# Kernel tuning notes

Measured on AMD Instinct MI355X. Metric: run time of the kernel, lower is better.

The kernel has to match this reference:

```python
import itertools
import jax, jax.numpy as jnp
import numpy as np

RES = 14
B = 64
DIM = 384
NH = 8
KD = 32
DV = 128  # attn_ratio * key_dim
SCALE = KD ** -0.5


def _bias_idxs(res):
    points = list(itertools.product(range(res), range(res)))
    offs, idxs = {}, []
    for p1 in points:
        for p2 in points:
            o = (abs(p1[0] - p2[0]), abs(p1[1] - p2[1]))
            if o not in offs:
                offs[o] = len(offs)
            idxs.append(offs[o])
    n = res * res
    return np.asarray(idxs, dtype=np.int32).reshape(n, n), len(offs)


def setup_inputs() -> dict:
    key = jax.random.key(0)
    ks = jax.random.split(key, 16)
    idxs, n_off = _bias_idxs(RES)  # n_off == 196 for res=14
    f = lambda k, shape, s=0.05: jax.random.normal(k, shape, dtype=jnp.float32) * s
    return {
        "x": jax.random.normal(ks[0], (B, DIM, RES, RES), dtype=jnp.float32),
        "qw": f(ks[1], (NH * KD, DIM)), "qb": f(ks[2], (NH * KD,)),
        "kw": f(ks[3], (NH * KD, DIM)), "kb": f(ks[4], (NH * KD,)),
        "vw": f(ks[5], (NH * DV, DIM)), "vb": f(ks[6], (NH * DV,)),
        "vlw": f(ks[7], (NH * DV, 1, 3, 3)), "vlb": f(ks[8], (NH * DV,)),
        "th1_w": f(ks[9], (NH, NH), 0.3), "th1_b": f(ks[10], (NH,)),
        "th2_w": f(ks[11], (NH, NH), 0.3), "th2_b": f(ks[12], (NH,)),
        "projw": f(ks[13], (DIM, NH * DV)), "projb": f(ks[14], (DIM,)),
        "bias_seg": f(ks[15], (NH, n_off), 0.5),
        "bias_idxs": jnp.asarray(idxs),
    }


def reference(x, qw, qb, kw, kb, vw, vb, vlw, vlb,
              th1_w, th1_b, th2_w, th2_b, projw, projb,
              bias_seg, bias_idxs):
    Bb, C, H, W = x.shape
    N = H * W
    xf = x.reshape(Bb, C, N)
    # 1x1 conv (+ folded BN) projections
    q = (jnp.einsum('oc,bcn->bon', qw, xf) + qb[:, None]).reshape(Bb, NH, KD, N).transpose(0, 1, 3, 2)  # [B,h,N,kd]
    k = (jnp.einsum('oc,bcn->bon', kw, xf) + kb[:, None]).reshape(Bb, NH, KD, N)                        # [B,h,kd,N]
    v4 = (jnp.einsum('oc,bcn->bon', vw, xf) + vb[:, None]).reshape(Bb, NH * DV, H, W)
    # depthwise 3x3 local branch (+ folded BN)
    v_local = jax.lax.conv_general_dilated(
        v4, vlw, window_strides=(1, 1), padding=[(1, 1), (1, 1)],
        dimension_numbers=('NCHW', 'OIHW', 'NCHW'), feature_group_count=NH * DV,
    ) + vlb[None, :, None, None]
    v = v4.reshape(Bb, NH, DV, N).transpose(0, 1, 3, 2)  # [B,h,N,dv]
    # attention scores + relative bias (bicubic interp 196->196 is identity)
    attn = jnp.einsum('bhnk,bhkm->bhnm', q, k) * SCALE
    bias = bias_seg[:, bias_idxs]  # [h,N,N]
    attn = attn + bias[None]
    # talking heads (1x1 conv over head dim) -> softmax -> talking heads
    attn = jnp.einsum('hg,bgnm->bhnm', th1_w, attn) + th1_b[None, :, None, None]
    attn = jax.nn.softmax(attn, axis=-1)
    attn = jnp.einsum('hg,bgnm->bhnm', th2_w, attn) + th2_b[None, :, None, None]
    o = jnp.einsum('bhnm,bhmd->bhnd', attn, v)           # [B,h,N,dv]
    o = o.transpose(0, 1, 3, 2).reshape(Bb, NH * DV, H, W) + v_local
    # proj: ReLU -> 1x1 conv (+ folded BN)
    o = jax.nn.relu(o)
    out = jnp.einsum('oc,bchw->bohw', projw, o) + projb[None, :, None, None]
    return out
```

## Files before the change

kernel.cpp:

```cpp
#include <hip/hip_runtime.h>
#include <hip/hip_bf16.h>


#define RES   14
#define NSP   196
#define NHD   8
#define KDIM  32
#define DVV   128
#define DIM   384
#define NQK   256
#define SCALE 0.17677669529663687f
#define SROW  224
#define NSTRIP 13

typedef __attribute__((ext_vector_type(8))) short bf16x8;
typedef __attribute__((ext_vector_type(4))) float f32x4;
typedef __attribute__((ext_vector_type(4))) unsigned short u16x4;
typedef unsigned short u16;
typedef unsigned int u32;

__device__ __forceinline__ u16 f2b(float f) {
    union { __hip_bfloat16 b; u16 u; } c; c.b = __float2bfloat16(f); return c.u;
}
__device__ __forceinline__ float b2f(u16 u) {
    union { __hip_bfloat16 b; u16 u; } c; c.u = u; return __bfloat162float(c.b);
}

__device__ __forceinline__ void gld16(const void* g, void* l) {
    __builtin_amdgcn_global_load_lds(
        (__attribute__((address_space(1))) void*)(unsigned long long)(const char*)g,
        (__attribute__((address_space(3))) void*)l, 16, 0, 0);
}

__device__ __forceinline__ void gemm128_bk64(const char* Aseg, long rbA,
                                             const char* Bseg, long rbB, int kIters,
                                             u16* A_lds, u16* B_lds, f32x4 acc[4][4])
{
    const int tid  = threadIdx.x;
    const int wid  = tid >> 6;
    const int lane = tid & 63;
    const int lrow = lane >> 2;
    const int lcb  = (lane & 3) << 4;
    const int r0   = wid * 32;
    const int wm   = (wid & 1) * 64, wn = (wid >> 1) * 64;
    const int l15  = lane & 15, lq8 = (lane >> 4) * 8;

    #pragma unroll
    for (int i = 0; i < 4; ++i)
        #pragma unroll
        for (int j = 0; j < 4; ++j) acc[i][j] = (f32x4){0.f, 0.f, 0.f, 0.f};

    const char* ap0 = Aseg + (long)(r0 + lrow) * rbA + lcb;
    const char* ap1 = ap0 + 16 * rbA;
    const char* bp0 = Bseg + (long)(r0 + lrow) * rbB + lcb;
    const char* bp1 = bp0 + 16 * rbB;
    u16* la0 = A_lds + r0 * 32;
    u16* la1 = la0 + 512;
    u16* lb0 = B_lds + r0 * 32;
    u16* lb1 = lb0 + 512;

    for (int kk = 0; kk < kIters; ++kk) {
        gld16(ap0, la0);        gld16(ap1, la1);
        gld16(bp0, lb0);        gld16(bp1, lb1);
        gld16(ap0 + 64, la0 + 4096); gld16(ap1 + 64, la1 + 4096);
        gld16(bp0 + 64, lb0 + 4096); gld16(bp1 + 64, lb1 + 4096);
        ap0 += 128; ap1 += 128; bp0 += 128; bp1 += 128;
        __syncthreads();
        #pragma unroll
        for (int s = 0; s < 2; ++s) {
            bf16x8 af[4], bfr[4];
            #pragma unroll
            for (int i = 0; i < 4; ++i)
                af[i] = *(const bf16x8*)&A_lds[s * 4096 + (wm + i * 16 + l15) * 32 + lq8];
            #pragma unroll
            for (int j = 0; j < 4; ++j)
                bfr[j] = *(const bf16x8*)&B_lds[s * 4096 + (wn + j * 16 + l15) * 32 + lq8];
            #pragma unroll
            for (int i = 0; i < 4; ++i)
                #pragma unroll
                for (int j = 0; j < 4; ++j)
                    acc[i][j] = __builtin_amdgcn_mfma_f32_16x16x32_bf16(
                        af[i], bfr[j], acc[i][j], 0, 0, 0);
        }
        __syncthreads();
    }
}

__global__ __launch_bounds__(256) void k_prep(
    const float* __restrict__ qw, const float* __restrict__ kw,
    const float* __restrict__ vw, const float* __restrict__ pw,
    const float* __restrict__ th1w, const float* __restrict__ th1b,
    const float* __restrict__ bias_seg, const float* __restrict__ vlw,
    const float* __restrict__ x,
    u16* __restrict__ wqkv, u16* __restrict__ pwb, float* __restrict__ biasmix,
    u16* __restrict__ wpack, u16* __restrict__ xb)
{
    __shared__ float t[32][33];
    const int bid = blockIdx.x;
    if (bid < 960) {
        const int i = (bid * 256 + threadIdx.x) * 4;
        const float* src; u16* dst;
        if (i < 98304)       { src = qw + i;            dst = wqkv + i; }
        else if (i < 196608) { src = kw + (i - 98304);  dst = wqkv + i; }
        else if (i < 589824) { src = vw + (i - 196608); dst = wqkv + i; }
        else                 { src = pw + (i - 589824); dst = pwb + (i - 589824); }
        float4 v = *(const float4*)src;
        u16x4 o;
        o[0] = f2b(v.x); o[1] = f2b(v.y); o[2] = f2b(v.z); o[3] = f2b(v.w);
        *(u16x4*)dst = o;
    } else if (bid == 960) {
        for (int i2 = threadIdx.x; i2 < 8 * NSP; i2 += 256) {
            int hh = i2 / NSP, off = i2 - hh * NSP;
            float a = th1b[hh];
            #pragma unroll
            for (int g = 0; g < 8; ++g) a += th1w[hh * 8 + g] * bias_seg[g * NSP + off];
            biasmix[i2] = a;
        }
    } else if (bid < 997) {
        int i2 = (bid - 961) * 256 + threadIdx.x;
        if (i2 < 9216) {
            int g = i2 / 72, r = i2 - g * 72;
            int tap = r >> 3, tt = r & 7;
            wpack[i2] = f2b(vlw[(g * 8 + tt) * 9 + tap]);
        }
    } else {
        const int L = bid - 997;
        const int b = L / 84, r = L - b * 84;
        const int c0 = (r / 7) * 32, n0 = (r % 7) * 32;
        const int tx = threadIdx.x & 31, ty = threadIdx.x >> 5;
        #pragma unroll
        for (int l = 0; l < 4; ++l) {
            int c = c0 + ty + 8 * l, n = n0 + tx;
            t[ty + 8 * l][tx] = (n < NSP) ? x[((long)b * DIM + c) * NSP + n] : 0.f;
        }
        __syncthreads();
        #pragma unroll
        for (int l = 0; l < 4; ++l) {
            int n = n0 + ty + 8 * l, c = c0 + tx;
            if (n < NSP) xb[((long)b * NSP + n) * DIM + c] = f2b(t[tx][ty + 8 * l]);
        }
    }
}

__global__ __launch_bounds__(256) void k_qkv(
    const u16* __restrict__ xb, const u16* __restrict__ wqkv,
    const float* __restrict__ qb, const float* __restrict__ kb,
    const float* __restrict__ vb,
    u16* __restrict__ qt, u16* __restrict__ kb16, u16* __restrict__ vt)
{
    __shared__ u16 A_lds[8192], B_lds[8192];
    const int m0 = blockIdx.x * 128, oc0 = blockIdx.y * 128;
    f32x4 acc[4][4];
    gemm128_bk64((const char*)xb + (long)m0 * 768, 768,
                 (const char*)wqkv + (long)oc0 * 768, 768, 6, A_lds, B_lds, acc);

    const int tid = threadIdx.x, wid = tid >> 6, lane = tid & 63;
    const int wm = (wid & 1) * 64, wn = (wid >> 1) * 64;
    const int col = lane & 15, quad = lane >> 4;
    #pragma unroll
    for (int i = 0; i < 4; ++i) {
        #pragma unroll
        for (int j = 0; j < 4; ++j) {
            #pragma unroll
            for (int r = 0; r < 4; ++r) {
                int m  = m0 + wm + i * 16 + quad * 4 + r;
                int oc = oc0 + wn + j * 16 + col;
                int b = m / NSP, n = m - b * NSP;
                float v = acc[i][j][r];
                if (oc < 256) {
                    qt[(long)m * NQK + oc] = f2b(v + qb[oc]);
                } else if (oc < 512) {
                    int o = oc - 256;
                    kb16[(long)m * NQK + o] = f2b(v + kb[o]);
                } else {
                    int o = oc - 512, h = o >> 7, d = o & 127;
                    vt[(((long)b * NHD + h) * NSP + n) * DVV + d] = f2b(v + vb[o]);
                }
            }
        }
    }
}

__global__ __launch_bounds__(256) void k_vtdw(
    const u16* __restrict__ vt, const u16* __restrict__ wpack,
    const float* __restrict__ vlb,
    u16* __restrict__ vtT, u16* __restrict__ vlt)
{
    __shared__ u16 t[32][33];
    const int bid = blockIdx.x;
    if (bid < 14336) {
        const int n_i = bid % 7;
        const int d_i = (bid / 7) & 3;
        const int bh  = bid / 28;
        const int d0 = d_i * 32, n0 = n_i * 32;
        const int tx = threadIdx.x & 31, ty = threadIdx.x >> 5;
        #pragma unroll
        for (int l = 0; l < 4; ++l) {
            int n = n0 + ty + 8 * l, d = d0 + tx;
            t[ty + 8 * l][tx] = (n < NSP) ? vt[((long)bh * NSP + n) * DVV + d] : (u16)0;
        }
        __syncthreads();
        #pragma unroll
        for (int l = 0; l < 4; ++l) {
            int d = d0 + ty + 8 * l, m = n0 + tx;
            vtT[((long)bh * DVV + d) * 224 + m] = t[tx][ty + 8 * l];
        }
    } else {
        const int b2 = bid - 14336;
        const int nx = b2 % 13;
        const int bh = b2 / 13;
        const int tid = threadIdx.x;
        const int dg = tid & 15;
        const int nl = tid >> 4;
        const int n  = nx * 16 + nl;
        if (n >= NSP) return;
        const int d0 = dg * 8;
        const int h  = bh & 7;
        const int y = n / RES, xx = n - y * RES;
        const long plane = (long)bh * NSP * DVV;
        float acc[8];
        #pragma unroll
        for (int k = 0; k < 8; ++k) acc[k] = vlb[h * DVV + d0 + k];
        const u16* wb = wpack + (h * 16 + dg) * 72;
        #pragma unroll
        for (int dy = -1; dy <= 1; ++dy) {
            int yy = y + dy;
            if (yy < 0 || yy >= RES) continue;
            #pragma unroll
            for (int dx = -1; dx <= 1; ++dx) {
                int xn = xx + dx;
                if (xn < 0 || xn >= RES) continue;
                int tap = (dy + 1) * 3 + dx + 1;
                bf16x8 v  = *(const bf16x8*)&vt[plane + (yy * RES + xn) * DVV + d0];
                bf16x8 wv = *(const bf16x8*)&wb[tap * 8];
                #pragma unroll
                for (int k = 0; k < 8; ++k)
                    acc[k] += b2f((u16)wv[k]) * b2f((u16)v[k]);
            }
        }
        bf16x8 r;
        #pragma unroll
        for (int k = 0; k < 8; ++k) r[k] = (short)f2b(acc[k]);
        *(bf16x8*)&vlt[plane + (long)n * DVV + d0] = r;
    }
}

__global__ __launch_bounds__(512, 2) void k_attn2(
    const u16* __restrict__ qt, const u16* __restrict__ kb16,
    const u16* __restrict__ vtT, const u16* __restrict__ vlt,
    const float* __restrict__ th1w, const float* __restrict__ th2w,
    const float* __restrict__ th2b, const float* __restrict__ biasmix,
    u16* __restrict__ ot)
{
    __shared__ u16 S[128 * SROW];
    __shared__ u16 bmS[8 * NSP];
    const int tid = threadIdx.x;
    const int L  = blockIdx.x;
    const int wq = L >> 3;
    const int b  = (L & 7) + ((wq / NSTRIP) << 3);
    const int n0 = (wq % NSTRIP) * 16;
    const int wid = tid >> 6, lane = tid & 63;
    const int l15 = lane & 15, lq8 = (lane >> 4) * 8;
    const int quad = lane >> 4, col = lane & 15;

    for (int i = tid; i < 8 * NSP; i += 512) bmS[i] = f2b(biasmix[i]);
    __syncthreads();

    {
        const long qrow = ((long)(b * NSP) + n0 + l15) * NQK;
        bf16x8 af[8];
        #pragma unroll
        for (int g = 0; g < 8; ++g)
            af[g] = *(const bf16x8*)&qt[qrow + g * 32 + lq8];
        #pragma unroll
        for (int jj = 0; jj < 2; ++jj) {
            const int j = wid + jj * 8;
            if (j >= 13) break;
            const long krow = ((long)(b * NSP) + j * 16 + l15) * NQK;
            f32x4 t[8];
            #pragma unroll
            for (int g = 0; g < 8; ++g) {
                bf16x8 bv = *(const bf16x8*)&kb16[krow + g * 32 + lq8];
                t[g] = __builtin_amdgcn_mfma_f32_16x16x32_bf16(
                    af[g], bv, (f32x4){0.f, 0.f, 0.f, 0.f}, 0, 0, 0);
            }
            const int m = j * 16 + col;
            const int ym = m / RES, xm = m - ym * RES;
            int offr[4];
            #pragma unroll
            for (int r = 0; r < 4; ++r) {
                int gn = n0 + quad * 4 + r;
                int yn = gn / RES, xn = gn - yn * RES;
                int off = abs(yn - ym) * RES + abs(xn - xm);
                offr[r] = (off > 195) ? 195 : off;
            }
            #pragma unroll
            for (int h = 0; h < 8; ++h) {
                float o[4];
                #pragma unroll
                for (int r = 0; r < 4; ++r) o[r] = b2f(bmS[h * NSP + offr[r]]);
                #pragma unroll
                for (int g = 0; g < 8; ++g) {
                    const float w = th1w[h * 8 + g] * SCALE;
                    #pragma unroll
                    for (int r = 0; r < 4; ++r) o[r] += w * t[g][r];
                }
                #pragma unroll
                for (int r = 0; r < 4; ++r)
                    S[(h * 16 + quad * 4 + r) * SROW + m] = f2b(o[r]);
            }
        }
    }
    __syncthreads();

    {
        const int c = lane & 15, rg = lane >> 4;
        #pragma unroll
        for (int it = 0; it < 4; ++it) {
            u16* row = &S[(wid * 16 + it * 4 + rg) * SROW];
            float v[13];
            #pragma unroll
            for (int k = 0; k < 12; ++k) v[k] = b2f(row[c + 16 * k]);
            v[12] = (c < 4) ? b2f(row[192 + c]) : -1e30f;
            float mx = v[0];
            #pragma unroll
            for (int k = 1; k < 13; ++k) mx = fmaxf(mx, v[k]);
            #pragma unroll
            for (int o = 1; o < 16; o <<= 1) mx = fmaxf(mx, __shfl_xor(mx, o));
            float sum = 0.f;
            #pragma unroll
            for (int k = 0; k < 13; ++k) { v[k] = __expf(v[k] - mx); sum += v[k]; }
            if (c >= 4) sum -= v[12];
            #pragma unroll
            for (int o = 1; o < 16; o <<= 1) sum += __shfl_xor(sum, o);
            float inv = 1.0f / sum;
            #pragma unroll
            for (int k = 0; k < 12; ++k) row[c + 16 * k] = f2b(v[k] * inv);
            if (c < 4) row[192 + c] = f2b(v[12] * inv);
        }
    }
    __syncthreads();

    {
        for (int p = tid; p < 16 * 112; p += 512) {
            const int nl = p / 112, kp = p - nl * 112;
            const int m0 = kp * 2;
            if (m0 >= NSP) {
                #pragma unroll
                for (int h = 0; h < 8; ++h)
                    *(u32*)&S[(h * 16 + nl) * SROW + m0] = 0u;
                continue;
            }
            float s0[8], s1[8];
            #pragma unroll
            for (int g = 0; g < 8; ++g) {
                u32 v = *(const u32*)&S[(g * 16 + nl) * SROW + m0];
                s0[g] = b2f((u16)(v & 0xffff));
                s1[g] = b2f((u16)(v >> 16));
            }
            #pragma unroll
            for (int h = 0; h < 8; ++h) {
                float o0 = th2b[h], o1 = th2b[h];
                #pragma unroll
                for (int g = 0; g < 8; ++g) {
                    const float w = th2w[h * 8 + g];
                    o0 += w * s0[g];
                    o1 += w * s1[g];
                }
                *(u32*)&S[(h * 16 + nl) * SROW + m0] =
                    (u32)f2b(o0) | ((u32)f2b(o1) << 16);
            }
        }
    }
    __syncthreads();

    {
        const int h = wid;
        const long vrow = (long)(b * NHD + h) * DVV;
        f32x4 acc[8];
        #pragma unroll
        for (int df = 0; df < 8; ++df) acc[df] = (f32x4){0.f, 0.f, 0.f, 0.f};
        for (int kc = 0; kc < 7; ++kc) {
            bf16x8 a0 = *(const bf16x8*)&S[(h * 16 + l15) * SROW + kc * 32 + lq8];
            #pragma unroll
            for (int df = 0; df < 8; ++df) {
                bf16x8 bv = *(const bf16x8*)&vtT[(vrow + df * 16 + l15) * 224 + kc * 32 + lq8];
                acc[df] = __builtin_amdgcn_mfma_f32_16x16x32_bf16(a0, bv, acc[df], 0, 0, 0);
            }
        }
        const long lbase = (long)(b * NHD + h) * NSP;
        #pragma unroll
        for (int df = 0; df < 8; ++df) {
            #pragma unroll
            for (int r = 0; r < 4; ++r) {
                int n = n0 + quad * 4 + r;
                int d = df * 16 + col;
                if (n < NSP) {
                    float v = acc[df][r] + b2f(vlt[(lbase + n) * DVV + d]);
                    v = fmaxf(v, 0.f);
                    ot[((long)(b * NSP + n)) * 1024 + h * DVV + d] = f2b(v);
                }
            }
        }
    }
}

__global__ __launch_bounds__(256) void k_proj(
    const u16* __restrict__ pwb, const u16* __restrict__ ot,
    const float* __restrict__ projb, float* __restrict__ outp)
{
    __shared__ u16 A_lds[8192];
    __shared__ u16 B_lds[4096];
    const int tid = threadIdx.x, wid = tid >> 6, lane = tid & 63;
    const int lrow = lane >> 2, lcb = (lane & 3) << 4;
    const int m0 = blockIdx.x * 64, oc0 = blockIdx.y * 128;
    const int wm = (wid & 1) * 64, wn = (wid >> 1) * 32;
    const int l15 = lane & 15, lq8 = (lane >> 4) * 8;

    const char* gp[6];
    u16* lp[6];
    #pragma unroll
    for (int t = 0; t < 6; ++t) {
        int s = wid * 6 + t;
        int sub = s / 12, s12 = s - sub * 12;
        if (s12 < 8) {
            gp[t] = (const char*)pwb + (long)(oc0 + s12 * 16 + lrow) * 2048 + lcb + sub * 64;
            lp[t] = A_lds + sub * 4096 + s12 * 512;
        } else {
            gp[t] = (const char*)ot + (long)(m0 + (s12 - 8) * 16 + lrow) * 2048 + lcb + sub * 64;
            lp[t] = B_lds + sub * 2048 + (s12 - 8) * 512;
        }
    }

    f32x4 acc[4][2];
    #pragma unroll
    for (int i = 0; i < 4; ++i)
        #pragma unroll
        for (int j = 0; j < 2; ++j) acc[i][j] = (f32x4){0.f, 0.f, 0.f, 0.f};

    for (int kk = 0; kk < 16; ++kk) {
        #pragma unroll
        for (int t = 0; t < 6; ++t) { gld16(gp[t], lp[t]); gp[t] += 128; }
        __syncthreads();
        #pragma unroll
        for (int s = 0; s < 2; ++s) {
            bf16x8 af[4], bfr[2];
            #pragma unroll
            for (int i = 0; i < 4; ++i)
                af[i] = *(const bf16x8*)&A_lds[s * 4096 + (wm + i * 16 + l15) * 32 + lq8];
            #pragma unroll
            for (int j = 0; j < 2; ++j)
                bfr[j] = *(const bf16x8*)&B_lds[s * 2048 + (wn + j * 16 + l15) * 32 + lq8];
            #pragma unroll
            for (int i = 0; i < 4; ++i)
                #pragma unroll
                for (int j = 0; j < 2; ++j)
                    acc[i][j] = __builtin_amdgcn_mfma_f32_16x16x32_bf16(
                        af[i], bfr[j], acc[i][j], 0, 0, 0);
        }
        __syncthreads();
    }

    const int col = lane & 15, quad = lane >> 4;
    #pragma unroll
    for (int i = 0; i < 4; ++i) {
        #pragma unroll
        for (int j = 0; j < 2; ++j) {
            #pragma unroll
            for (int r = 0; r < 4; ++r) {
                int oc = oc0 + wm + i * 16 + quad * 4 + r;
                int mg = m0 + wn + j * 16 + col;
                int b = mg / NSP, n = mg - b * NSP;
                outp[((long)b * DIM + oc) * NSP + n] = acc[i][j][r] + projb[oc];
            }
        }
    }
}

extern "C" void kernel_launch(void* const* d_in, const int* in_sizes, int n_in,
                              void* d_out, int out_size, void* d_ws, size_t ws_size,
                              hipStream_t stream) {
    const float* x        = (const float*)d_in[0];
    const float* qw       = (const float*)d_in[1];
    const float* qb       = (const float*)d_in[2];
    const float* kw       = (const float*)d_in[3];
    const float* kb       = (const float*)d_in[4];
    const float* vw       = (const float*)d_in[5];
    const float* vb       = (const float*)d_in[6];
    const float* vlw      = (const float*)d_in[7];
    const float* vlb      = (const float*)d_in[8];
    const float* th1w     = (const float*)d_in[9];
    const float* th1b     = (const float*)d_in[10];
    const float* th2w     = (const float*)d_in[11];
    const float* th2b     = (const float*)d_in[12];
    const float* projw    = (const float*)d_in[13];
    const float* projb    = (const float*)d_in[14];
    const float* bias_seg = (const float*)d_in[15];
    float* outp = (float*)d_out;

    char* w = (char*)d_ws;
    u16* xb      = (u16*)(w);
    u16* wqkv    = (u16*)(w + 9633792);
    u16* pwb     = (u16*)(w + 10813440);
    u16* wpack   = (u16*)(w + 11599872);
    float* bmix  = (float*)(w + 11618304);
    u16* qt      = (u16*)(w + 11624704);
    u16* kb16    = (u16*)(w + 18080000);
    u16* vt      = (u16*)(w + 24535296);
    u16* vtT     = (u16*)(w + 50225408);
    u16* ot      = (u16*)(w + 79585536);
    u16* vlt     = (u16*)(w + 105275648);

    k_prep<<<dim3(6373), 256, 0, stream>>>(qw, kw, vw, projw, th1w, th1b,
                                           bias_seg, vlw, x, wqkv, pwb, bmix,
                                           wpack, xb);
    k_qkv<<<dim3(98, 12), 256, 0, stream>>>(xb, wqkv, qb, kb, vb, qt, kb16, vt);
    k_vtdw<<<dim3(20992), 256, 0, stream>>>(vt, wpack, vlb, vtT, vlt);
    k_attn2<<<dim3(NSTRIP * 64), 512, 0, stream>>>(qt, kb16, vtT, vlt, th1w, th2w,
                                                   th2b, bmix, ot);
    k_proj<<<dim3(196, 3), 256, 0, stream>>>(pwb, ot, projb, outp);
}
```

Before: 291.2 us.

## Fuse output projection into attention kernel via LDS-staged activations

The separate projection GEMM kernel is removed. Each attention block now writes its ReLU'd 16-row output tile (all 8 heads) into shared memory and multiplies it by the projection weights read straight from global memory, writing the final fp32 output. This drops the bf16 intermediate round trip through global memory and one kernel launch. In exchange, each block re-reads the full 384x1024 projection weight, the output tile is only 16 rows wide so MFMA reuse is low, and an extra barrier is added.

Measured after the change: 338.7 us. +16.3%, slower.

```diff
diff --git a/kernel.cpp b/kernel.cpp
--- a/kernel.cpp
+++ b/kernel.cpp
@@ -11,6 +11,7 @@
 #define NQK   256
 #define SCALE 0.17677669529663687f
 #define SROW  224
+#define OROW  1032
 #define NSTRIP 13
 
 typedef __attribute__((ext_vector_type(8))) short bf16x8;
@@ -250,7 +251,8 @@
     const u16* __restrict__ vtT, const u16* __restrict__ vlt,
     const float* __restrict__ th1w, const float* __restrict__ th2w,
     const float* __restrict__ th2b, const float* __restrict__ biasmix,
-    u16* __restrict__ ot)
+    const u16* __restrict__ pwb, const float* __restrict__ projb,
+    float* __restrict__ outp)
 {
     __shared__ u16 S[128 * SROW];
     __shared__ u16 bmS[8 * NSP];
@@ -388,90 +390,42 @@
                 acc[df] = __builtin_amdgcn_mfma_f32_16x16x32_bf16(a0, bv, acc[df], 0, 0, 0);
             }
         }
+        __syncthreads();
         const long lbase = (long)(b * NHD + h) * NSP;
         #pragma unroll
         for (int df = 0; df < 8; ++df) {
+            const int d = df * 16 + col;
             #pragma unroll
             for (int r = 0; r < 4; ++r) {
-                int n = n0 + quad * 4 + r;
-                int d = df * 16 + col;
-                if (n < NSP) {
-                    float v = acc[df][r] + b2f(vlt[(lbase + n) * DVV + d]);
-                    v = fmaxf(v, 0.f);
-                    ot[((long)(b * NSP + n)) * 1024 + h * DVV + d] = f2b(v);
+                const int nl = quad * 4 + r;
+                const int n = n0 + nl;
+                const int nn = (n < NSP) ? n : (NSP - 1);
+                float v = acc[df][r] + b2f(vlt[(lbase + nn) * DVV + d]);
+                S[nl * OROW + h * 128 + d] = f2b(fmaxf(v, 0.f));
+            }
+        }
+    }
+    __syncthreads();
+
+    {
+        const int n = n0 + col;
+        #pragma unroll
+        for (int t = 0; t < 3; ++t) {
+            const int ocb = wid * 48 + t * 16;
+            const long arow = (long)(ocb + l15) * 1024 + lq8;
+            f32x4 pacc = (f32x4){0.f, 0.f, 0.f, 0.f};
+            #pragma unroll 8
+            for (int kk = 0; kk < 32; ++kk) {
+                bf16x8 af = *(const bf16x8*)&pwb[arow + kk * 32];
+                bf16x8 bv = *(const bf16x8*)&S[l15 * OROW + kk * 32 + lq8];
+                pacc = __builtin_amdgcn_mfma_f32_16x16x32_bf16(af, bv, pacc, 0, 0, 0);
+            }
+            if (n < NSP) {
+                #pragma unroll
+                for (int r = 0; r < 4; ++r) {
+                    const int oc = ocb + quad * 4 + r;
+                    outp[((long)b * DIM + oc) * NSP + n] = pacc[r] + projb[oc];
                 }
-            }
-        }
-    }
-}
-
-__global__ __launch_bounds__(256) void k_proj(
-    const u16* __restrict__ pwb, const u16* __restrict__ ot,
-    const float* __restrict__ projb, float* __restrict__ outp)
-{
-    __shared__ u16 A_lds[8192];
-    __shared__ u16 B_lds[4096];
-    const int tid = threadIdx.x, wid = tid >> 6, lane = tid & 63;
-    const int lrow = lane >> 2, lcb = (lane & 3) << 4;
-    const int m0 = blockIdx.x * 64, oc0 = blockIdx.y * 128;
-    const int wm = (wid & 1) * 64, wn = (wid >> 1) * 32;
-    const int l15 = lane & 15, lq8 = (lane >> 4) * 8;
-
-    const char* gp[6];
-    u16* lp[6];
-    #pragma unroll
-    for (int t = 0; t < 6; ++t) {
-        int s = wid * 6 + t;
-        int sub = s / 12, s12 = s - sub * 12;
-        if (s12 < 8) {
-            gp[t] = (const char*)pwb + (long)(oc0 + s12 * 16 + lrow) * 2048 + lcb + sub * 64;
-            lp[t] = A_lds + sub * 4096 + s12 * 512;
-        } else {
-            gp[t] = (const char*)ot + (long)(m0 + (s12 - 8) * 16 + lrow) * 2048 + lcb + sub * 64;
-            lp[t] = B_lds + sub * 2048 + (s12 - 8) * 512;
-        }
-    }
-
-    f32x4 acc[4][2];
-    #pragma unroll
-    for (int i = 0; i < 4; ++i)
-        #pragma unroll
-        for (int j = 0; j < 2; ++j) acc[i][j] = (f32x4){0.f, 0.f, 0.f, 0.f};
-
-    for (int kk = 0; kk < 16; ++kk) {
-        #pragma unroll
-        for (int t = 0; t < 6; ++t) { gld16(gp[t], lp[t]); gp[t] += 128; }
-        __syncthreads();
-        #pragma unroll
-        for (int s = 0; s < 2; ++s) {
-            bf16x8 af[4], bfr[2];
-            #pragma unroll
-            for (int i = 0; i < 4; ++i)
-                af[i] = *(const bf16x8*)&A_lds[s * 4096 + (wm + i * 16 + l15) * 32 + lq8];
-            #pragma unroll
-            for (int j = 0; j < 2; ++j)
-                bfr[j] = *(const bf16x8*)&B_lds[s * 2048 + (wn + j * 16 + l15) * 32 + lq8];
-            #pragma unroll
-            for (int i = 0; i < 4; ++i)
-                #pragma unroll
-                for (int j = 0; j < 2; ++j)
-                    acc[i][j] = __builtin_amdgcn_mfma_f32_16x16x32_bf16(
-                        af[i], bfr[j], acc[i][j], 0, 0, 0);
-        }
-        __syncthreads();
-    }
-
-    const int col = lane & 15, quad = lane >> 4;
-    #pragma unroll
-    for (int i = 0; i < 4; ++i) {
-        #pragma unroll
-        for (int j = 0; j < 2; ++j) {
-            #pragma unroll
-            for (int r = 0; r < 4; ++r) {
-                int oc = oc0 + wm + i * 16 + quad * 4 + r;
-                int mg = m0 + wn + j * 16 + col;
-                int b = mg / NSP, n = mg - b * NSP;
-                outp[((long)b * DIM + oc) * NSP + n] = acc[i][j][r] + projb[oc];
             }
         }
     }
@@ -508,7 +462,6 @@
     u16* kb16    = (u16*)(w + 18080000);
     u16* vt      = (u16*)(w + 24535296);
     u16* vtT     = (u16*)(w + 50225408);
-    u16* ot      = (u16*)(w + 79585536);
     u16* vlt     = (u16*)(w + 105275648);
 
     k_prep<<<dim3(6373), 256, 0, stream>>>(qw, kw, vw, projw, th1w, th1b,
@@ -517,6 +470,5 @@
     k_qkv<<<dim3(98, 12), 256, 0, stream>>>(xb, wqkv, qb, kb, vb, qt, kb16, vt);
     k_vtdw<<<dim3(20992), 256, 0, stream>>>(vt, wpack, vlb, vtT, vlt);
     k_attn2<<<dim3(NSTRIP * 64), 512, 0, stream>>>(qt, kb16, vtT, vlt, th1w, th2w,
-                                                   th2b, bmix, ot);
-    k_proj<<<dim3(196, 3), 256, 0, stream>>>(pwb, ot, projb, outp);
-}
+                                                   th2b, bmix, pwb, projb, outp);
+}
```

## Merge V transpose and depthwise conv into one block per batch-head plane

Applied to the files above, without the earlier changes.

The transpose/depthwise kernel now launches one block per (batch, head). Each block loads the whole 196x128 V plane into padded LDS once, writes the transposed copy from LDS with vector stores, and computes the 3x3 depthwise conv from LDS with the 9 tap weights held in registers. This removes the separate 32x32 transpose tiles and the repeated global reads of neighbour taps across thousands of small blocks. The cost is a much smaller grid of 512 blocks with about 53KB of LDS each, which lowers occupancy, and the transpose reads columns out of LDS, which may cause bank conflicts.

Measured after the change: 281.7 us. -3.2%, faster.

```diff
diff --git a/kernel.cpp b/kernel.cpp
--- a/kernel.cpp
+++ b/kernel.cpp
@@ -11,6 +11,7 @@
 #define NQK   256
 #define SCALE 0.17677669529663687f
 #define SROW  224
+#define PROW  136
 #define NSTRIP 13
 
 typedef __attribute__((ext_vector_type(8))) short bf16x8;
@@ -186,62 +187,79 @@
     const float* __restrict__ vlb,
     u16* __restrict__ vtT, u16* __restrict__ vlt)
 {
-    __shared__ u16 t[32][33];
-    const int bid = blockIdx.x;
-    if (bid < 14336) {
-        const int n_i = bid % 7;
-        const int d_i = (bid / 7) & 3;
-        const int bh  = bid / 28;
-        const int d0 = d_i * 32, n0 = n_i * 32;
-        const int tx = threadIdx.x & 31, ty = threadIdx.x >> 5;
-        #pragma unroll
-        for (int l = 0; l < 4; ++l) {
-            int n = n0 + ty + 8 * l, d = d0 + tx;
-            t[ty + 8 * l][tx] = (n < NSP) ? vt[((long)bh * NSP + n) * DVV + d] : (u16)0;
-        }
-        __syncthreads();
-        #pragma unroll
-        for (int l = 0; l < 4; ++l) {
-            int d = d0 + ty + 8 * l, m = n0 + tx;
-            vtT[((long)bh * DVV + d) * 224 + m] = t[tx][ty + 8 * l];
-        }
-    } else {
-        const int b2 = bid - 14336;
-        const int nx = b2 % 13;
-        const int bh = b2 / 13;
-        const int tid = threadIdx.x;
-        const int dg = tid & 15;
-        const int nl = tid >> 4;
-        const int n  = nx * 16 + nl;
-        if (n >= NSP) return;
+    __shared__ u16 P[NSP * PROW];
+    const int bh = blockIdx.x;
+    const int tid = threadIdx.x;
+    const int h = bh & 7;
+    const long plane = (long)bh * NSP * DVV;
+
+    {
+        const int dseg = tid & 15, nrow = tid >> 4;
+        #pragma unroll
+        for (int i = 0; i < 13; ++i) {
+            int n = i * 16 + nrow;
+            if (n < NSP)
+                *(bf16x8*)&P[n * PROW + dseg * 8] =
+                    *(const bf16x8*)&vt[plane + (long)n * DVV + dseg * 8];
+        }
+    }
+    __syncthreads();
+
+    {
+        const int d = tid >> 1, half = tid & 1;
+        const long orow = ((long)bh * DVV + d) * 224;
+        #pragma unroll
+        for (int k = 0; k < 14; ++k) {
+            const int nb = half * 112 + k * 8;
+            u16 tmp[8];
+            #pragma unroll
+            for (int j = 0; j < 8; ++j) {
+                int n = nb + j;
+                tmp[j] = (n < NSP) ? P[n * PROW + d] : (u16)0;
+            }
+            *(u16x4*)&vtT[orow + nb]     = *(u16x4*)&tmp[0];
+            *(u16x4*)&vtT[orow + nb + 4] = *(u16x4*)&tmp[4];
+        }
+    }
+
+    {
+        const int dg = tid & 15, nl = tid >> 4;
         const int d0 = dg * 8;
-        const int h  = bh & 7;
-        const int y = n / RES, xx = n - y * RES;
-        const long plane = (long)bh * NSP * DVV;
-        float acc[8];
-        #pragma unroll
-        for (int k = 0; k < 8; ++k) acc[k] = vlb[h * DVV + d0 + k];
         const u16* wb = wpack + (h * 16 + dg) * 72;
-        #pragma unroll
-        for (int dy = -1; dy <= 1; ++dy) {
-            int yy = y + dy;
-            if (yy < 0 || yy >= RES) continue;
-            #pragma unroll
-            for (int dx = -1; dx <= 1; ++dx) {
-                int xn = xx + dx;
-                if (xn < 0 || xn >= RES) continue;
-                int tap = (dy + 1) * 3 + dx + 1;
-                bf16x8 v  = *(const bf16x8*)&vt[plane + (yy * RES + xn) * DVV + d0];
-                bf16x8 wv = *(const bf16x8*)&wb[tap * 8];
-                #pragma unroll
-                for (int k = 0; k < 8; ++k)
-                    acc[k] += b2f((u16)wv[k]) * b2f((u16)v[k]);
-            }
-        }
-        bf16x8 r;
-        #pragma unroll
-        for (int k = 0; k < 8; ++k) r[k] = (short)f2b(acc[k]);
-        *(bf16x8*)&vlt[plane + (long)n * DVV + d0] = r;
+        bf16x8 wv[9];
+        #pragma unroll
+        for (int tap = 0; tap < 9; ++tap) wv[tap] = *(const bf16x8*)&wb[tap * 8];
+        float bias[8];
+        #pragma unroll
+        for (int k2 = 0; k2 < 8; ++k2) bias[k2] = vlb[h * DVV + d0 + k2];
+        #pragma unroll
+        for (int c = 0; c < 13; ++c) {
+            const int n = c * 16 + nl;
+            if (n >= NSP) break;
+            const int y = n / RES, xx = n - y * RES;
+            float acc[8];
+            #pragma unroll
+            for (int k2 = 0; k2 < 8; ++k2) acc[k2] = bias[k2];
+            #pragma unroll
+            for (int dy = -1; dy <= 1; ++dy) {
+                int yy = y + dy;
+                if (yy < 0 || yy >= RES) continue;
+                #pragma unroll
+                for (int dx = -1; dx <= 1; ++dx) {
+                    int xn = xx + dx;
+                    if (xn < 0 || xn >= RES) continue;
+                    int tap = (dy + 1) * 3 + dx + 1;
+                    bf16x8 v = *(const bf16x8*)&P[(yy * RES + xn) * PROW + d0];
+                    #pragma unroll
+                    for (int k2 = 0; k2 < 8; ++k2)
+                        acc[k2] += b2f((u16)wv[tap][k2]) * b2f((u16)v[k2]);
+                }
+            }
+            bf16x8 r;
+            #pragma unroll
+            for (int k2 = 0; k2 < 8; ++k2) r[k2] = (short)f2b(acc[k2]);
+            *(bf16x8*)&vlt[plane + (long)n * DVV + d0] = r;
+        }
     }
 }
 
@@ -515,7 +533,7 @@
                                            bias_seg, vlw, x, wqkv, pwb, bmix,
                                            wpack, xb);
     k_qkv<<<dim3(98, 12), 256, 0, stream>>>(xb, wqkv, qb, kb, vb, qt, kb16, vt);
-    k_vtdw<<<dim3(20992), 256, 0, stream>>>(vt, wpack, vlb, vtT, vlt);
+    k_vtdw<<<dim3(512), 256, 0, stream>>>(vt, wpack, vlb, vtT, vlt);
     k_attn2<<<dim3(NSTRIP * 64), 512, 0, stream>>>(qt, kb16, vtT, vlt, th1w, th2w,
                                                    th2b, bmix, ot);
     k_proj<<<dim3(196, 3), 256, 0, stream>>>(pwb, ot, projb, outp);
```
